# Kernel optimization log

Hardware: AMD Instinct MI355X
Metric: run time of the kernel (lower is better)

Reference implementation:

```python
import jax, jax.numpy as jnp
import numpy as np

N_NODES = 50000


def graph_conv(src, dst, x, W, b, n_nodes):
    """DGL GraphConv, norm='both': D_out^{-1/2} A D_in^{-1/2} x W + b.
    src/dst: [E] edge endpoints (message flows src -> dst).
    """
    ones = jnp.ones(src.shape[0], dtype=x.dtype)
    deg_out = jnp.clip(jax.ops.segment_sum(ones, src, num_segments=n_nodes), 1.0)
    deg_in = jnp.clip(jax.ops.segment_sum(ones, dst, num_segments=n_nodes), 1.0)
    h = x * jax.lax.rsqrt(deg_out)[:, None]          # src-side normalization
    msgs = h[src]                                     # [E, F] gather (irregular)
    agg = jax.ops.segment_sum(msgs, dst, num_segments=n_nodes)  # SpMM scatter-add
    agg = agg * jax.lax.rsqrt(deg_in)[:, None]        # dst-side normalization
    return agg @ W + b


def setup_inputs() -> dict:
    key = jax.random.key(0)
    ks = jax.random.split(key, 9)
    E = 600000
    in_f, hid, emb = 128, 64, 32
    features = jax.random.normal(ks[0], (N_NODES, in_f), dtype=jnp.float32)
    src = jax.random.randint(ks[1], (E,), 0, N_NODES)
    dst = jax.random.randint(ks[2], (E,), 0, N_NODES)

    def glorot(k, fan_in, fan_out):
        lim = np.sqrt(6.0 / (fan_in + fan_out)).astype(np.float32)
        return jax.random.uniform(k, (fan_in, fan_out), jnp.float32, -lim, lim)

    return {
        "features": features, "src": src, "dst": dst,
        "W1": glorot(ks[3], in_f, hid), "b1": jnp.zeros((hid,), jnp.float32),
        "W2": glorot(ks[4], hid, emb), "b2": jnp.zeros((emb,), jnp.float32),
        "W3": glorot(ks[5], emb, in_f), "b3": jnp.zeros((in_f,), jnp.float32),
    }


def reference(features, src, dst, W1, b1, W2, b2, W3, b3):
    h = jax.nn.relu(graph_conv(src, dst, features, W1, b1, N_NODES))
    z = graph_conv(src, dst, h, W2, b2, N_NODES)
    recon = graph_conv(src, dst, z, W3, b3, N_NODES)
    return (z, recon)
```

## Files before the change

### kernel.cpp

```cpp
#include <hip/hip_runtime.h>
#include <hip/hip_bf16.h>


#define HNB 4
#define HPB 64
#define HBIN 12500
typedef unsigned short u16;

__device__ __forceinline__ float bfhi(unsigned u) {
    unsigned v = u & 0xFFFF0000u;
    return __builtin_bit_cast(float, v);
}
__device__ __forceinline__ float bflo(unsigned u) {
    unsigned v = u << 16;
    return __builtin_bit_cast(float, v);
}
__device__ __forceinline__ unsigned f2bf(float f) {
    unsigned u = __builtin_bit_cast(unsigned, f);
    return (u + 0x7FFFu + ((u >> 16) & 1u)) >> 16;
}

__global__ __launch_bounds__(256) void k_hist2(
    const int* __restrict__ src, const int* __restrict__ dst,
    u16* __restrict__ slab, int E, int slice)
{
    __shared__ int h[HBIN];
    const int which = blockIdx.x / (HNB * HPB);
    const int bin   = (blockIdx.x / HPB) % HNB;
    const int p     = blockIdx.x % HPB;
    const int* __restrict__ idx = which ? dst : src;

    for (int i = threadIdx.x; i < HBIN; i += 256) h[i] = 0;
    __syncthreads();

    const int lo  = bin * HBIN;
    const int beg = p * slice;
    const int fin = min(beg + slice, E);
    for (int i = beg + threadIdx.x * 4; i + 3 < fin; i += 1024) {
        const int4 v = *(const int4*)(idx + i);
        int u;
        u = v.x - lo; if ((unsigned)u < (unsigned)HBIN) atomicAdd(&h[u], 1);
        u = v.y - lo; if ((unsigned)u < (unsigned)HBIN) atomicAdd(&h[u], 1);
        u = v.z - lo; if ((unsigned)u < (unsigned)HBIN) atomicAdd(&h[u], 1);
        u = v.w - lo; if ((unsigned)u < (unsigned)HBIN) atomicAdd(&h[u], 1);
    }
    for (int i = beg + ((fin - beg) & ~3) + threadIdx.x; i < fin; i += 256) {
        int u = idx[i] - lo;
        if ((unsigned)u < (unsigned)HBIN) atomicAdd(&h[u], 1);
    }
    __syncthreads();

    unsigned* out = (unsigned*)(slab + (size_t)blockIdx.x * HBIN);
    for (int i = threadIdx.x; i < HBIN / 2; i += 256)
        out[i] = (unsigned)h[2 * i] | ((unsigned)h[2 * i + 1] << 16);
}

__global__ __launch_bounds__(256) void k_reduce2(
    u16* __restrict__ slab, int* __restrict__ cnt_in,
    float* __restrict__ rs_out, float* __restrict__ rs_in, int N)
{
    const int i = blockIdx.x * 256 + threadIdx.x;
    if (i >= N) return;
    const int bin = i / HBIN;
    const int off = i - bin * HBIN;

    const u16* s_src = slab + ((size_t)(bin * HPB)) * HBIN + off;
    u16*       s_dst = slab + ((size_t)((HNB + bin) * HPB)) * HBIN + off;

    int so = 0;
#pragma unroll
    for (int p = 0; p < HPB; ++p) so += s_src[(size_t)p * HBIN];

    int run = 0;
#pragma unroll
    for (int p = 0; p < HPB; ++p) {
        const int c = s_dst[(size_t)p * HBIN];
        s_dst[(size_t)p * HBIN] = (u16)run;
        run += c;
    }
    cnt_in[i] = run;
    rs_out[i] = rsqrtf(fmaxf((float)so, 1.0f));
    rs_in[i]  = rsqrtf(fmaxf((float)run, 1.0f));
}

__global__ void k_scan1(const int* __restrict__ cnt, int* __restrict__ partial,
                        int* __restrict__ blocksum, int n) {
    __shared__ int tmp[256];
    const int tid = threadIdx.x;
    const int i = blockIdx.x * 256 + tid;
    int v = (i < n) ? cnt[i] : 0;
    tmp[tid] = v; __syncthreads();
    for (int off = 1; off < 256; off <<= 1) {
        int t = (tid >= off) ? tmp[tid - off] : 0;
        __syncthreads(); tmp[tid] += t; __syncthreads();
    }
    if (i < n) partial[i] = tmp[tid];
    if (tid == 255) blocksum[blockIdx.x] = tmp[255];
}

__global__ void k_scan2(int* __restrict__ blocksum, int nb) {
    __shared__ int tmp[256];
    const int tid = threadIdx.x;
    int v = (tid < nb) ? blocksum[tid] : 0;
    tmp[tid] = v; __syncthreads();
    for (int off = 1; off < 256; off <<= 1) {
        int t = (tid >= off) ? tmp[tid - off] : 0;
        __syncthreads(); tmp[tid] += t; __syncthreads();
    }
    if (tid < nb) blocksum[tid] = tmp[tid];
}

__global__ void k_scan3(const int* __restrict__ partial, const int* __restrict__ blocksum,
                        int* __restrict__ row_ptr, int n) {
    const int i = blockIdx.x * 256 + threadIdx.x;
    if (i < n) {
        const int base = (blockIdx.x > 0) ? blocksum[blockIdx.x - 1] : 0;
        row_ptr[i + 1] = partial[i] + base;
        if (i == 0) row_ptr[0] = 0;
    }
}

__global__ __launch_bounds__(256) void k_fill2(
    const int* __restrict__ src, const int* __restrict__ dst,
    const int* __restrict__ row_ptr, const u16* __restrict__ slab,
    int* __restrict__ csr_src, int E, int slice, int N)
{
    __shared__ int cur[HBIN];
    const int bin = blockIdx.x / HPB;
    const int p   = blockIdx.x % HPB;
    const int lo  = bin * HBIN;

    const u16* part_off = slab + ((size_t)((HNB + bin) * HPB + p)) * HBIN;
    for (int j = threadIdx.x; j < HBIN; j += 256) {
        const int node = lo + j;
        cur[j] = (node < N) ? (row_ptr[node] + (int)part_off[j]) : 0;
    }
    __syncthreads();

    const int beg = p * slice;
    const int fin = min(beg + slice, E);
    for (int i = beg + threadIdx.x * 4; i + 3 < fin; i += 1024) {
        const int4 d = *(const int4*)(dst + i);
        const int4 s = *(const int4*)(src + i);
        int u;
        u = d.x - lo; if ((unsigned)u < (unsigned)HBIN) csr_src[atomicAdd(&cur[u], 1)] = s.x;
        u = d.y - lo; if ((unsigned)u < (unsigned)HBIN) csr_src[atomicAdd(&cur[u], 1)] = s.y;
        u = d.z - lo; if ((unsigned)u < (unsigned)HBIN) csr_src[atomicAdd(&cur[u], 1)] = s.z;
        u = d.w - lo; if ((unsigned)u < (unsigned)HBIN) csr_src[atomicAdd(&cur[u], 1)] = s.w;
    }
    for (int i = beg + ((fin - beg) & ~3) + threadIdx.x; i < fin; i += 256) {
        int u = dst[i] - lo;
        if ((unsigned)u < (unsigned)HBIN) csr_src[atomicAdd(&cur[u], 1)] = src[i];
    }
}

template <int IN_F, int OUT_F, int TM, bool OUT_BF16>
__global__ __launch_bounds__(256) void k_gemm_tiled(
    const float* __restrict__ X, const float* __restrict__ W,
    const float* __restrict__ rowscale, const float* __restrict__ bias,
    void* __restrict__ Y, int n)
{
    constexpr int CT  = OUT_F / 4;
    constexpr int RT  = 256 / CT;
    constexpr int RPT = TM / RT;
    constexpr int XS  = IN_F + 4;
    __shared__ float sW[IN_F * OUT_F];
    __shared__ float sX[TM * XS];
    const int tid = threadIdx.x;
    const int row0 = blockIdx.x * TM;

    for (int i = tid; i < IN_F * OUT_F / 4; i += 256)
        ((float4*)sW)[i] = ((const float4*)W)[i];
    for (int i = tid; i < TM * IN_F / 4; i += 256) {
        const int r  = i / (IN_F / 4);
        const int c4 = (i % (IN_F / 4)) * 4;
        const int gr = row0 + r;
        float4 v = make_float4(0.f, 0.f, 0.f, 0.f);
        if (gr < n) v = *(const float4*)(X + (long)gr * IN_F + c4);
        *(float4*)(sX + r * XS + c4) = v;
    }
    __syncthreads();

    const int tc = tid % CT;
    const int tr = tid / CT;
    float4 acc[RPT];
#pragma unroll
    for (int i = 0; i < RPT; ++i) acc[i] = make_float4(0.f, 0.f, 0.f, 0.f);

#pragma unroll 8
    for (int k = 0; k < IN_F; ++k) {
        const float4 w = *(const float4*)(sW + k * OUT_F + 4 * tc);
#pragma unroll
        for (int i = 0; i < RPT; ++i) {
            const float xv = sX[(tr + i * RT) * XS + k];
            acc[i].x += xv * w.x; acc[i].y += xv * w.y;
            acc[i].z += xv * w.z; acc[i].w += xv * w.w;
        }
    }

#pragma unroll
    for (int i = 0; i < RPT; ++i) {
        const int gr = row0 + tr + i * RT;
        if (gr < n) {
            float4 v = acc[i];
            if (rowscale) {
                const float s = rowscale[gr];
                v.x *= s; v.y *= s; v.z *= s; v.w *= s;
            }
            if (bias) {
                const float4 bb = *(const float4*)(bias + 4 * tc);
                v.x += bb.x; v.y += bb.y; v.z += bb.z; v.w += bb.w;
            }
            if (OUT_BF16) {
                uint2 pk;
                pk.x = f2bf(v.x) | (f2bf(v.y) << 16);
                pk.y = f2bf(v.z) | (f2bf(v.w) << 16);
                *(uint2*)((u16*)Y + (size_t)gr * OUT_F + 4 * tc) = pk;
            } else {
                *(float4*)((float*)Y + (size_t)gr * OUT_F + 4 * tc) = v;
            }
        }
    }
}

template <int F, bool RELU, bool HAS_BIAS, bool SHADOW>
__global__ __launch_bounds__(256) void k_gather_b(
    const int* __restrict__ row_ptr, const int* __restrict__ csr_src,
    const u16* __restrict__ Xb, const float* __restrict__ rs_in,
    const float* __restrict__ rs_sh, const float* __restrict__ bias,
    float* __restrict__ O, u16* __restrict__ Osh, int N)
{
    constexpr int L   = F / 8;
    constexpr int NPB = 256 / L;
    const int node = blockIdx.x * NPB + threadIdx.x / L;
    const int c8 = (threadIdx.x % L) * 8;
    if (node >= N) return;

    const int beg = row_ptr[node];
    const int end = row_ptr[node + 1];
    float a[8];
#pragma unroll
    for (int t = 0; t < 8; ++t) a[t] = 0.f;

    int j = beg;
    for (; j + 3 < end; j += 4) {
        const int s0 = csr_src[j], s1 = csr_src[j + 1];
        const int s2 = csr_src[j + 2], s3 = csr_src[j + 3];
        const uint4 q0 = *(const uint4*)(Xb + (size_t)s0 * F + c8);
        const uint4 q1 = *(const uint4*)(Xb + (size_t)s1 * F + c8);
        const uint4 q2 = *(const uint4*)(Xb + (size_t)s2 * F + c8);
        const uint4 q3 = *(const uint4*)(Xb + (size_t)s3 * F + c8);
        a[0] += bflo(q0.x); a[1] += bfhi(q0.x); a[2] += bflo(q0.y); a[3] += bfhi(q0.y);
        a[4] += bflo(q0.z); a[5] += bfhi(q0.z); a[6] += bflo(q0.w); a[7] += bfhi(q0.w);
        a[0] += bflo(q1.x); a[1] += bfhi(q1.x); a[2] += bflo(q1.y); a[3] += bfhi(q1.y);
        a[4] += bflo(q1.z); a[5] += bfhi(q1.z); a[6] += bflo(q1.w); a[7] += bfhi(q1.w);
        a[0] += bflo(q2.x); a[1] += bfhi(q2.x); a[2] += bflo(q2.y); a[3] += bfhi(q2.y);
        a[4] += bflo(q2.z); a[5] += bfhi(q2.z); a[6] += bflo(q2.w); a[7] += bfhi(q2.w);
        a[0] += bflo(q3.x); a[1] += bfhi(q3.x); a[2] += bflo(q3.y); a[3] += bfhi(q3.y);
        a[4] += bflo(q3.z); a[5] += bfhi(q3.z); a[6] += bflo(q3.w); a[7] += bfhi(q3.w);
    }
    for (; j < end; ++j) {
        const int s = csr_src[j];
        const uint4 q = *(const uint4*)(Xb + (size_t)s * F + c8);
        a[0] += bflo(q.x); a[1] += bfhi(q.x); a[2] += bflo(q.y); a[3] += bfhi(q.y);
        a[4] += bflo(q.z); a[5] += bfhi(q.z); a[6] += bflo(q.w); a[7] += bfhi(q.w);
    }

    const float rs = rs_in[node];
    float v[8];
#pragma unroll
    for (int t = 0; t < 8; ++t) v[t] = a[t] * rs;
    if (HAS_BIAS) {
        const float4 b0 = *(const float4*)(bias + c8);
        const float4 b1 = *(const float4*)(bias + c8 + 4);
        v[0] += b0.x; v[1] += b0.y; v[2] += b0.z; v[3] += b0.w;
        v[4] += b1.x; v[5] += b1.y; v[6] += b1.z; v[7] += b1.w;
    }
    if (RELU) {
#pragma unroll
        for (int t = 0; t < 8; ++t) v[t] = fmaxf(v[t], 0.f);
    }
    float* o = O + (size_t)node * F + c8;
    *(float4*)(o)     = make_float4(v[0], v[1], v[2], v[3]);
    *(float4*)(o + 4) = make_float4(v[4], v[5], v[6], v[7]);

    if (SHADOW) {
        const float ss = rs_sh[node];
        uint4 pk;
        pk.x = f2bf(v[0] * ss) | (f2bf(v[1] * ss) << 16);
        pk.y = f2bf(v[2] * ss) | (f2bf(v[3] * ss) << 16);
        pk.z = f2bf(v[4] * ss) | (f2bf(v[5] * ss) << 16);
        pk.w = f2bf(v[6] * ss) | (f2bf(v[7] * ss) << 16);
        *(uint4*)(Osh + (size_t)node * F + c8) = pk;
    }
}

extern "C" void kernel_launch(void* const* d_in, const int* in_sizes, int n_in,
                              void* d_out, int out_size, void* d_ws, size_t ws_size,
                              hipStream_t stream) {
    const float* feat = (const float*)d_in[0];
    const int*   src  = (const int*)d_in[1];
    const int*   dst  = (const int*)d_in[2];
    const float* W1   = (const float*)d_in[3];
    const float* b1   = (const float*)d_in[4];
    const float* W2   = (const float*)d_in[5];
    const float* b2   = (const float*)d_in[6];
    const float* W3   = (const float*)d_in[7];
    const float* b3   = (const float*)d_in[8];

    const int E = in_sizes[1];
    const int N = in_sizes[0] / 128;
    const int slice = (((E + HPB - 1) / HPB) + 3) & ~3;

    const size_t SLABN = 2UL * HNB * HPB * HBIN;
    u16* slab     = (u16*)d_ws;
    int* row_ptr  = (int*)(slab + SLABN);
    int* scan_p   = row_ptr + N + 16;
    int* blocksum = scan_p + N;
    int* cnt_in   = blocksum + 256;
    int* csr_src  = cnt_in + N;
    float* rs_out = (float*)(csr_src + E);
    float* rs_in  = rs_out + N;
    float* h1     = rs_in + N;
    u16* t2b      = (u16*)(h1 + (size_t)N * 64);
    u16* zb       = t2b + (size_t)N * 32;
    float* agg3   = (float*)(zb + (size_t)N * 32);
    u16* t1b      = (u16*)slab;

    float* z_out  = (float*)d_out;
    float* recon  = z_out + (size_t)N * 32;

    const int B = 256;
    const int nb_scan = (N + 255) / 256;

    k_hist2<<<2 * HNB * HPB, B, 0, stream>>>(src, dst, slab, E, slice);
    k_reduce2<<<nb_scan, B, 0, stream>>>(slab, cnt_in, rs_out, rs_in, N);
    k_scan1<<<nb_scan, B, 0, stream>>>(cnt_in, scan_p, blocksum, N);
    k_scan2<<<1, B, 0, stream>>>(blocksum, nb_scan);
    k_scan3<<<nb_scan, B, 0, stream>>>(scan_p, blocksum, row_ptr, N);
    k_fill2<<<HNB * HPB, B, 0, stream>>>(src, dst, row_ptr, slab, csr_src, E, slice, N);

    k_gemm_tiled<128, 64, 32, true><<<(N + 31) / 32, B, 0, stream>>>(
        feat, W1, rs_out, nullptr, t1b, N);
    k_gather_b<64, true, true, false><<<(N + 31) / 32, B, 0, stream>>>(
        row_ptr, csr_src, t1b, rs_in, nullptr, b1, h1, nullptr, N);

    k_gemm_tiled<64, 32, 64, true><<<(N + 63) / 64, B, 0, stream>>>(
        h1, W2, rs_out, nullptr, t2b, N);
    k_gather_b<32, false, true, true><<<(N + 63) / 64, B, 0, stream>>>(
        row_ptr, csr_src, t2b, rs_in, rs_out, b2, z_out, zb, N);

    k_gather_b<32, false, false, false><<<(N + 63) / 64, B, 0, stream>>>(
        row_ptr, csr_src, zb, rs_in, nullptr, nullptr, agg3, nullptr, N);
    k_gemm_tiled<32, 128, 64, false><<<(N + 63) / 64, B, 0, stream>>>(
        agg3, W3, nullptr, b3, recon, N);
}
```

Baseline: 223.1 us.

## Fuse gather with following dense GEMMs and merge reduce with scan

Merges the degree reduction kernel with the first scan pass, fuses the layer-1 aggregation (bias+ReLU) with the W2 GEMM via shared memory, and fuses the layer-3 aggregation with the W3 GEMM plus bias. This removes the fp32 intermediates h1 and agg3 round-tripping through global memory and cuts three kernel launches. The fused kernels carry extra shared memory and load the weight tile per block, which may lower occupancy during the latency-bound gather phase.

```diff
diff --git a/kernel.cpp b/kernel.cpp
--- a/kernel.cpp
+++ b/kernel.cpp
@@ -55,46 +55,39 @@
         out[i] = (unsigned)h[2 * i] | ((unsigned)h[2 * i + 1] << 16);
 }
 
-__global__ __launch_bounds__(256) void k_reduce2(
-    u16* __restrict__ slab, int* __restrict__ cnt_in,
-    float* __restrict__ rs_out, float* __restrict__ rs_in, int N)
-{
-    const int i = blockIdx.x * 256 + threadIdx.x;
-    if (i >= N) return;
-    const int bin = i / HBIN;
-    const int off = i - bin * HBIN;
-
-    const u16* s_src = slab + ((size_t)(bin * HPB)) * HBIN + off;
-    u16*       s_dst = slab + ((size_t)((HNB + bin) * HPB)) * HBIN + off;
-
-    int so = 0;
-#pragma unroll
-    for (int p = 0; p < HPB; ++p) so += s_src[(size_t)p * HBIN];
-
-    int run = 0;
-#pragma unroll
-    for (int p = 0; p < HPB; ++p) {
-        const int c = s_dst[(size_t)p * HBIN];
-        s_dst[(size_t)p * HBIN] = (u16)run;
-        run += c;
-    }
-    cnt_in[i] = run;
-    rs_out[i] = rsqrtf(fmaxf((float)so, 1.0f));
-    rs_in[i]  = rsqrtf(fmaxf((float)run, 1.0f));
-}
-
-__global__ void k_scan1(const int* __restrict__ cnt, int* __restrict__ partial,
-                        int* __restrict__ blocksum, int n) {
+__global__ __launch_bounds__(256) void k_reduce_scan(
+    u16* __restrict__ slab, float* __restrict__ rs_out, float* __restrict__ rs_in,
+    int* __restrict__ partial, int* __restrict__ blocksum, int N)
+{
     __shared__ int tmp[256];
     const int tid = threadIdx.x;
     const int i = blockIdx.x * 256 + tid;
-    int v = (i < n) ? cnt[i] : 0;
-    tmp[tid] = v; __syncthreads();
+
+    int run = 0;
+    if (i < N) {
+        const int bin = i / HBIN;
+        const int off = i - bin * HBIN;
+        const u16* s_src = slab + ((size_t)(bin * HPB)) * HBIN + off;
+        u16*       s_dst = slab + ((size_t)((HNB + bin) * HPB)) * HBIN + off;
+
+        int so = 0;
+#pragma unroll
+        for (int p = 0; p < HPB; ++p) so += s_src[(size_t)p * HBIN];
+#pragma unroll
+        for (int p = 0; p < HPB; ++p) {
+            const int c = s_dst[(size_t)p * HBIN];
+            s_dst[(size_t)p * HBIN] = (u16)run;
+            run += c;
+        }
+        rs_out[i] = rsqrtf(fmaxf((float)so, 1.0f));
+        rs_in[i]  = rsqrtf(fmaxf((float)run, 1.0f));
+    }
+    tmp[tid] = run; __syncthreads();
     for (int off = 1; off < 256; off <<= 1) {
         int t = (tid >= off) ? tmp[tid - off] : 0;
         __syncthreads(); tmp[tid] += t; __syncthreads();
     }
-    if (i < n) partial[i] = tmp[tid];
+    if (i < N) partial[i] = tmp[tid];
     if (tid == 255) blocksum[blockIdx.x] = tmp[255];
 }
 
@@ -154,11 +147,10 @@
     }
 }
 
-template <int IN_F, int OUT_F, int TM, bool OUT_BF16>
-__global__ __launch_bounds__(256) void k_gemm_tiled(
+template <int IN_F, int OUT_F, int TM>
+__global__ __launch_bounds__(256) void k_gemm_bf16out(
     const float* __restrict__ X, const float* __restrict__ W,
-    const float* __restrict__ rowscale, const float* __restrict__ bias,
-    void* __restrict__ Y, int n)
+    const float* __restrict__ rowscale, u16* __restrict__ Y, int n)
 {
     constexpr int CT  = OUT_F / 4;
     constexpr int RT  = 256 / CT;
@@ -203,37 +195,99 @@
         const int gr = row0 + tr + i * RT;
         if (gr < n) {
             float4 v = acc[i];
-            if (rowscale) {
-                const float s = rowscale[gr];
-                v.x *= s; v.y *= s; v.z *= s; v.w *= s;
-            }
-            if (bias) {
-                const float4 bb = *(const float4*)(bias + 4 * tc);
-                v.x += bb.x; v.y += bb.y; v.z += bb.z; v.w += bb.w;
-            }
-            if (OUT_BF16) {
-                uint2 pk;
-                pk.x = f2bf(v.x) | (f2bf(v.y) << 16);
-                pk.y = f2bf(v.z) | (f2bf(v.w) << 16);
-                *(uint2*)((u16*)Y + (size_t)gr * OUT_F + 4 * tc) = pk;
-            } else {
-                *(float4*)((float*)Y + (size_t)gr * OUT_F + 4 * tc) = v;
-            }
-        }
-    }
-}
-
-template <int F, bool RELU, bool HAS_BIAS, bool SHADOW>
-__global__ __launch_bounds__(256) void k_gather_b(
+            const float s = rowscale[gr];
+            v.x *= s; v.y *= s; v.z *= s; v.w *= s;
+            uint2 pk;
+            pk.x = f2bf(v.x) | (f2bf(v.y) << 16);
+            pk.y = f2bf(v.z) | (f2bf(v.w) << 16);
+            *(uint2*)(Y + (size_t)gr * OUT_F + 4 * tc) = pk;
+        }
+    }
+}
+
+__global__ __launch_bounds__(256) void k_gather_gemm_B(
     const int* __restrict__ row_ptr, const int* __restrict__ csr_src,
-    const u16* __restrict__ Xb, const float* __restrict__ rs_in,
-    const float* __restrict__ rs_sh, const float* __restrict__ bias,
-    float* __restrict__ O, u16* __restrict__ Osh, int N)
-{
-    constexpr int L   = F / 8;
-    constexpr int NPB = 256 / L;
-    const int node = blockIdx.x * NPB + threadIdx.x / L;
-    const int c8 = (threadIdx.x % L) * 8;
+    const u16* __restrict__ t1b, const float* __restrict__ rs_in,
+    const float* __restrict__ rs_out, const float* __restrict__ b1,
+    const float* __restrict__ W2, u16* __restrict__ t2b, int N)
+{
+    __shared__ float sh[32][72];
+    __shared__ float sW[64 * 32];
+    const int tid = threadIdx.x;
+
+    for (int i = tid; i < 64 * 32 / 4; i += 256)
+        ((float4*)sW)[i] = ((const float4*)W2)[i];
+
+    const int nloc = tid / 8;
+    const int node = blockIdx.x * 32 + nloc;
+    const int c8 = (tid % 8) * 8;
+
+    float a[8];
+#pragma unroll
+    for (int t = 0; t < 8; ++t) a[t] = 0.f;
+
+    if (node < N) {
+        const int beg = row_ptr[node];
+        const int end = row_ptr[node + 1];
+        int j = beg;
+        for (; j + 3 < end; j += 4) {
+            const int s0 = csr_src[j], s1 = csr_src[j + 1];
+            const int s2 = csr_src[j + 2], s3 = csr_src[j + 3];
+            const uint4 q0 = *(const uint4*)(t1b + (size_t)s0 * 64 + c8);
+            const uint4 q1 = *(const uint4*)(t1b + (size_t)s1 * 64 + c8);
+            const uint4 q2 = *(const uint4*)(t1b + (size_t)s2 * 64 + c8);
+            const uint4 q3 = *(const uint4*)(t1b + (size_t)s3 * 64 + c8);
+            a[0] += bflo(q0.x); a[1] += bfhi(q0.x); a[2] += bflo(q0.y); a[3] += bfhi(q0.y);
+            a[4] += bflo(q0.z); a[5] += bfhi(q0.z); a[6] += bflo(q0.w); a[7] += bfhi(q0.w);
+            a[0] += bflo(q1.x); a[1] += bfhi(q1.x); a[2] += bflo(q1.y); a[3] += bfhi(q1.y);
+            a[4] += bflo(q1.z); a[5] += bfhi(q1.z); a[6] += bflo(q1.w); a[7] += bfhi(q1.w);
+            a[0] += bflo(q2.x); a[1] += bfhi(q2.x); a[2] += bflo(q2.y); a[3] += bfhi(q2.y);
+            a[4] += bflo(q2.z); a[5] += bfhi(q2.z); a[6] += bflo(q2.w); a[7] += bfhi(q2.w);
+            a[0] += bflo(q3.x); a[1] += bfhi(q3.x); a[2] += bflo(q3.y); a[3] += bfhi(q3.y);
+            a[4] += bflo(q3.z); a[5] += bfhi(q3.z); a[6] += bflo(q3.w); a[7] += bfhi(q3.w);
+        }
+        for (; j < end; ++j) {
+            const int s = csr_src[j];
+            const uint4 q = *(const uint4*)(t1b + (size_t)s * 64 + c8);
+            a[0] += bflo(q.x); a[1] += bfhi(q.x); a[2] += bflo(q.y); a[3] += bfhi(q.y);
+            a[4] += bflo(q.z); a[5] += bfhi(q.z); a[6] += bflo(q.w); a[7] += bfhi(q.w);
+        }
+        const float rs = rs_in[node];
+#pragma unroll
+        for (int t = 0; t < 8; ++t)
+            a[t] = fmaxf(a[t] * rs + b1[c8 + t], 0.f);
+    }
+#pragma unroll
+    for (int t = 0; t < 8; ++t) sh[nloc][c8 + t] = a[t];
+    __syncthreads();
+
+    const int n2 = tid / 8;
+    const int c4 = (tid % 8) * 4;
+    float4 acc = make_float4(0.f, 0.f, 0.f, 0.f);
+#pragma unroll 8
+    for (int k = 0; k < 64; ++k) {
+        const float xv = sh[n2][k];
+        const float4 w = *(const float4*)(sW + k * 32 + c4);
+        acc.x += xv * w.x; acc.y += xv * w.y; acc.z += xv * w.z; acc.w += xv * w.w;
+    }
+    const int gn = blockIdx.x * 32 + n2;
+    if (gn < N) {
+        const float s = rs_out[gn];
+        uint2 pk;
+        pk.x = f2bf(acc.x * s) | (f2bf(acc.y * s) << 16);
+        pk.y = f2bf(acc.z * s) | (f2bf(acc.w * s) << 16);
+        *(uint2*)(t2b + (size_t)gn * 32 + c4) = pk;
+    }
+}
+
+__global__ __launch_bounds__(256) void k_gather_C(
+    const int* __restrict__ row_ptr, const int* __restrict__ csr_src,
+    const u16* __restrict__ t2b, const float* __restrict__ rs_in,
+    const float* __restrict__ rs_out, const float* __restrict__ b2,
+    float* __restrict__ z, u16* __restrict__ zb, int N)
+{
+    const int node = blockIdx.x * 64 + threadIdx.x / 4;
+    const int c8 = (threadIdx.x % 4) * 8;
     if (node >= N) return;
 
     const int beg = row_ptr[node];
@@ -246,10 +300,10 @@
     for (; j + 3 < end; j += 4) {
         const int s0 = csr_src[j], s1 = csr_src[j + 1];
         const int s2 = csr_src[j + 2], s3 = csr_src[j + 3];
-        const uint4 q0 = *(const uint4*)(Xb + (size_t)s0 * F + c8);
-        const uint4 q1 = *(const uint4*)(Xb + (size_t)s1 * F + c8);
-        const uint4 q2 = *(const uint4*)(Xb + (size_t)s2 * F + c8);
-        const uint4 q3 = *(const uint4*)(Xb + (size_t)s3 * F + c8);
+        const uint4 q0 = *(const uint4*)(t2b + (size_t)s0 * 32 + c8);
+        const uint4 q1 = *(const uint4*)(t2b + (size_t)s1 * 32 + c8);
+        const uint4 q2 = *(const uint4*)(t2b + (size_t)s2 * 32 + c8);
+        const uint4 q3 = *(const uint4*)(t2b + (size_t)s3 * 32 + c8);
         a[0] += bflo(q0.x); a[1] += bfhi(q0.x); a[2] += bflo(q0.y); a[3] += bfhi(q0.y);
         a[4] += bflo(q0.z); a[5] += bfhi(q0.z); a[6] += bflo(q0.w); a[7] += bfhi(q0.w);
         a[0] += bflo(q1.x); a[1] += bfhi(q1.x); a[2] += bflo(q1.y); a[3] += bfhi(q1.y);
@@ -261,7 +315,7 @@
     }
     for (; j < end; ++j) {
         const int s = csr_src[j];
-        const uint4 q = *(const uint4*)(Xb + (size_t)s * F + c8);
+        const uint4 q = *(const uint4*)(t2b + (size_t)s * 32 + c8);
         a[0] += bflo(q.x); a[1] += bfhi(q.x); a[2] += bflo(q.y); a[3] += bfhi(q.y);
         a[4] += bflo(q.z); a[5] += bfhi(q.z); a[6] += bflo(q.w); a[7] += bfhi(q.w);
     }
@@ -269,29 +323,96 @@
     const float rs = rs_in[node];
     float v[8];
 #pragma unroll
-    for (int t = 0; t < 8; ++t) v[t] = a[t] * rs;
-    if (HAS_BIAS) {
-        const float4 b0 = *(const float4*)(bias + c8);
-        const float4 b1 = *(const float4*)(bias + c8 + 4);
-        v[0] += b0.x; v[1] += b0.y; v[2] += b0.z; v[3] += b0.w;
-        v[4] += b1.x; v[5] += b1.y; v[6] += b1.z; v[7] += b1.w;
-    }
-    if (RELU) {
-#pragma unroll
-        for (int t = 0; t < 8; ++t) v[t] = fmaxf(v[t], 0.f);
-    }
-    float* o = O + (size_t)node * F + c8;
+    for (int t = 0; t < 8; ++t) v[t] = a[t] * rs + b2[c8 + t];
+
+    float* o = z + (size_t)node * 32 + c8;
     *(float4*)(o)     = make_float4(v[0], v[1], v[2], v[3]);
     *(float4*)(o + 4) = make_float4(v[4], v[5], v[6], v[7]);
 
-    if (SHADOW) {
-        const float ss = rs_sh[node];
-        uint4 pk;
-        pk.x = f2bf(v[0] * ss) | (f2bf(v[1] * ss) << 16);
-        pk.y = f2bf(v[2] * ss) | (f2bf(v[3] * ss) << 16);
-        pk.z = f2bf(v[4] * ss) | (f2bf(v[5] * ss) << 16);
-        pk.w = f2bf(v[6] * ss) | (f2bf(v[7] * ss) << 16);
-        *(uint4*)(Osh + (size_t)node * F + c8) = pk;
+    const float ss = rs_out[node];
+    uint4 pk;
+    pk.x = f2bf(v[0] * ss) | (f2bf(v[1] * ss) << 16);
+    pk.y = f2bf(v[2] * ss) | (f2bf(v[3] * ss) << 16);
+    pk.z = f2bf(v[4] * ss) | (f2bf(v[5] * ss) << 16);
+    pk.w = f2bf(v[6] * ss) | (f2bf(v[7] * ss) << 16);
+    *(uint4*)(zb + (size_t)node * 32 + c8) = pk;
+}
+
+__global__ __launch_bounds__(256) void k_gather_gemm_D(
+    const int* __restrict__ row_ptr, const int* __restrict__ csr_src,
+    const u16* __restrict__ zb, const float* __restrict__ rs_in,
+    const float* __restrict__ W3, const float* __restrict__ b3,
+    float* __restrict__ recon, int N)
+{
+    __shared__ float sa[64][36];
+    __shared__ float sW[32 * 128];
+    const int tid = threadIdx.x;
+
+    for (int i = tid; i < 32 * 128 / 4; i += 256)
+        ((float4*)sW)[i] = ((const float4*)W3)[i];
+
+    const int nloc = tid / 4;
+    const int node = blockIdx.x * 64 + nloc;
+    const int c8 = (tid % 4) * 8;
+
+    float a[8];
+#pragma unroll
+    for (int t = 0; t < 8; ++t) a[t] = 0.f;
+
+    if (node < N) {
+        const int beg = row_ptr[node];
+        const int end = row_ptr[node + 1];
+        int j = beg;
+        for (; j + 3 < end; j += 4) {
+            const int s0 = csr_src[j], s1 = csr_src[j + 1];
+            const int s2 = csr_src[j + 2], s3 = csr_src[j + 3];
+            const uint4 q0 = *(const uint4*)(zb + (size_t)s0 * 32 + c8);
+            const uint4 q1 = *(const uint4*)(zb + (size_t)s1 * 32 + c8);
+            const uint4 q2 = *(const uint4*)(zb + (size_t)s2 * 32 + c8);
+            const uint4 q3 = *(const uint4*)(zb + (size_t)s3 * 32 + c8);
+            a[0] += bflo(q0.x); a[1] += bfhi(q0.x); a[2] += bflo(q0.y); a[3] += bfhi(q0.y);
+            a[4] += bflo(q0.z); a[5] += bfhi(q0.z); a[6] += bflo(q0.w); a[7] += bfhi(q0.w);
+            a[0] += bflo(q1.x); a[1] += bfhi(q1.x); a[2] += bflo(q1.y); a[3] += bfhi(q1.y);
+            a[4] += bflo(q1.z); a[5] += bfhi(q1.z); a[6] += bflo(q1.w); a[7] += bfhi(q1.w);
+            a[0] += bflo(q2.x); a[1] += bfhi(q2.x); a[2] += bflo(q2.y); a[3] += bfhi(q2.y);
+            a[4] += bflo(q2.z); a[5] += bfhi(q2.z); a[6] += bflo(q2.w); a[7] += bfhi(q2.w);
+            a[0] += bflo(q3.x); a[1] += bfhi(q3.x); a[2] += bflo(q3.y); a[3] += bfhi(q3.y);
+            a[4] += bflo(q3.z); a[5] += bfhi(q3.z); a[6] += bflo(q3.w); a[7] += bfhi(q3.w);
+        }
+        for (; j < end; ++j) {
+            const int s = csr_src[j];
+            const uint4 q = *(const uint4*)(zb + (size_t)s * 32 + c8);
+            a[0] += bflo(q.x); a[1] += bfhi(q.x); a[2] += bflo(q.y); a[3] += bfhi(q.y);
+            a[4] += bflo(q.z); a[5] += bfhi(q.z); a[6] += bflo(q.w); a[7] += bfhi(q.w);
+        }
+        const float rs = rs_in[node];
+#pragma unroll
+        for (int t = 0; t < 8; ++t) a[t] *= rs;
+    }
+#pragma unroll
+    for (int t = 0; t < 8; ++t) sa[nloc][c8 + t] = a[t];
+    __syncthreads();
+
+    const int ng = (tid / 32) * 8;
+    const int c4 = (tid % 32) * 4;
+    const float4 bb = *(const float4*)(b3 + c4);
+    float4 acc[8];
+#pragma unroll
+    for (int i = 0; i < 8; ++i) acc[i] = bb;
+#pragma unroll 4
+    for (int k = 0; k < 32; ++k) {
+        const float4 w = *(const float4*)(sW + k * 128 + c4);
+#pragma unroll
+        for (int i = 0; i < 8; ++i) {
+            const float xv = sa[ng + i][k];
+            acc[i].x += xv * w.x; acc[i].y += xv * w.y;
+            acc[i].z += xv * w.z; acc[i].w += xv * w.w;
+        }
+    }
+#pragma unroll
+    for (int i = 0; i < 8; ++i) {
+        const int gn = blockIdx.x * 64 + ng + i;
+        if (gn < N) *(float4*)(recon + (size_t)gn * 128 + c4) = acc[i];
     }
 }
 
@@ -317,14 +438,11 @@
     int* row_ptr  = (int*)(slab + SLABN);
     int* scan_p   = row_ptr + N + 16;
     int* blocksum = scan_p + N;
-    int* cnt_in   = blocksum + 256;
-    int* csr_src  = cnt_in + N;
+    int* csr_src  = blocksum + 256;
     float* rs_out = (float*)(csr_src + E);
     float* rs_in  = rs_out + N;
-    float* h1     = rs_in + N;
-    u16* t2b      = (u16*)(h1 + (size_t)N * 64);
+    u16* t2b      = (u16*)(rs_in + N);
     u16* zb       = t2b + (size_t)N * 32;
-    float* agg3   = (float*)(zb + (size_t)N * 32);
     u16* t1b      = (u16*)slab;
 
     float* z_out  = (float*)d_out;
@@ -334,24 +452,20 @@
     const int nb_scan = (N + 255) / 256;
 
     k_hist2<<<2 * HNB * HPB, B, 0, stream>>>(src, dst, slab, E, slice);
-    k_reduce2<<<nb_scan, B, 0, stream>>>(slab, cnt_in, rs_out, rs_in, N);
-    k_scan1<<<nb_scan, B, 0, stream>>>(cnt_in, scan_p, blocksum, N);
+    k_reduce_scan<<<nb_scan, B, 0, stream>>>(slab, rs_out, rs_in, scan_p, blocksum, N);
     k_scan2<<<1, B, 0, stream>>>(blocksum, nb_scan);
     k_scan3<<<nb_scan, B, 0, stream>>>(scan_p, blocksum, row_ptr, N);
     k_fill2<<<HNB * HPB, B, 0, stream>>>(src, dst, row_ptr, slab, csr_src, E, slice, N);
 
-    k_gemm_tiled<128, 64, 32, true><<<(N + 31) / 32, B, 0, stream>>>(
-        feat, W1, rs_out, nullptr, t1b, N);
-    k_gather_b<64, true, true, false><<<(N + 31) / 32, B, 0, stream>>>(
-        row_ptr, csr_src, t1b, rs_in, nullptr, b1, h1, nullptr, N);
-
-    k_gemm_tiled<64, 32, 64, true><<<(N + 63) / 64, B, 0, stream>>>(
-        h1, W2, rs_out, nullptr, t2b, N);
-    k_gather_b<32, false, true, true><<<(N + 63) / 64, B, 0, stream>>>(
+    k_gemm_bf16out<128, 64, 32><<<(N + 31) / 32, B, 0, stream>>>(
+        feat, W1, rs_out, t1b, N);
+
+    k_gather_gemm_B<<<(N + 31) / 32, B, 0, stream>>>(
+        row_ptr, csr_src, t1b, rs_in, rs_out, b1, W2, t2b, N);
+
+    k_gather_C<<<(N + 63) / 64, B, 0, stream>>>(
         row_ptr, csr_src, t2b, rs_in, rs_out, b2, z_out, zb, N);
 
-    k_gather_b<32, false, false, false><<<(N + 63) / 64, B, 0, stream>>>(
-        row_ptr, csr_src, zb, rs_in, nullptr, nullptr, agg3, nullptr, N);
-    k_gemm_tiled<32, 128, 64, false><<<(N + 63) / 64, B, 0, stream>>>(
-        agg3, W3, nullptr, b3, recon, N);
-}
+    k_gather_gemm_D<<<(N + 63) / 64, B, 0, stream>>>(
+        row_ptr, csr_src, zb, rs_in, W3, b3, recon, N);
+}
```

Measured after the change: 212.7 us. 4.7% less time.
